# Performance work log

Measured on AMD Instinct MI355X. Metric: run time of the kernel, lower is better.

Reference implementation:

```python
import jax, jax.numpy as jnp
import numpy as np

T = 5
EPS = 1e-05
G = 4      # num_groups
D = 64     # num_channels per group


def setup_inputs() -> dict:
    key = jax.random.key(0)
    X = jax.random.normal(key, (32, 256, 56, 56), dtype=jnp.float32)
    weight = jnp.ones((1, 256, 1, 1), dtype=jnp.float32)
    bias = jnp.zeros((1, 256, 1, 1), dtype=jnp.float32)
    return {"X": X, "weight": weight, "bias": bias}


def reference(X, weight, bias):
    N, C, H, W = X.shape
    # (N,C,H,W) -> (C,N,H,W) -> (g, d, m) with m = N*H*W
    x = X.transpose(1, 0, 2, 3).reshape(G, D, -1)
    m = x.shape[-1]
    mean = x.mean(-1, keepdims=True)                 # (g, d, 1)
    xc = x - mean
    I = jnp.eye(D, dtype=X.dtype)
    # Sigma = eps*I + xc xc^T / m     (g, d, d)
    Sigma = EPS * I + jnp.einsum('gdm,gem->gde', xc, xc) / m
    # trace normalization
    rTr = 1.0 / jnp.trace(Sigma, axis1=1, axis2=2)[:, None, None]  # (g,1,1)
    Sn = Sigma * rTr
    # Newton-Schulz iterations: P_{k+1} = 1.5 P_k - 0.5 P_k^3 Sn
    P = jnp.broadcast_to(I, (G, D, D))
    for _ in range(T):
        P = 1.5 * P - 0.5 * (P @ P @ P @ Sn)
    wm = P * jnp.sqrt(rTr)                           # whitening matrix (g,d,d)
    xn = wm @ xc                                     # (g, d, m)
    Xh = xn.reshape(C, N, H, W).transpose(1, 0, 2, 3)
    return Xh * weight + bias
```

## Files before the change

kernel.cpp:

```cpp
#include <hip/hip_runtime.h>
#include <math.h>

#define GROUPS 4
#define DCH    64
#define NBATCH 32
#define CTOT   256
#define HW     3136
#define CHW    (CTOT*HW)
#define MTOT   (NBATCH*HW)
#define PB     196
#define EPSV   1e-5f

typedef __attribute__((ext_vector_type(8))) short bf16x8;
typedef __attribute__((ext_vector_type(4))) float f32x4;

__device__ __forceinline__ f32x4 mfma16(bf16x8 a, bf16x8 b, f32x4 c) {
    return __builtin_amdgcn_mfma_f32_16x16x32_bf16(a, b, c, 0, 0, 0);
}

__device__ __forceinline__ void split2(float x, short& h, short& l) {
    union { float f; unsigned u; } c; c.f = x;
    h = (short)(c.u >> 16);
    union { unsigned u; float f; } hm; hm.u = c.u & 0xFFFF0000u;
    union { float f; unsigned u; } lo; lo.f = x - hm.f;
    l = (short)(lo.u >> 16);
}

__device__ __forceinline__ void load_slab(const float* bp, float dst[16]) {
    float4 a0 = *reinterpret_cast<const float4*>(bp);
    float4 a1 = *reinterpret_cast<const float4*>(bp + 4);
    float4 b0 = *reinterpret_cast<const float4*>(bp + 32);
    float4 b1 = *reinterpret_cast<const float4*>(bp + 36);
    dst[0]=a0.x; dst[1]=a0.y; dst[2]=a0.z;  dst[3]=a0.w;
    dst[4]=a1.x; dst[5]=a1.y; dst[6]=a1.z;  dst[7]=a1.w;
    dst[8]=b0.x; dst[9]=b0.y; dst[10]=b0.z; dst[11]=b0.w;
    dst[12]=b1.x; dst[13]=b1.y; dst[14]=b1.z; dst[15]=b1.w;
}

__global__ __launch_bounds__(512) void k1_gram(const float* __restrict__ X,
                                               float* __restrict__ pGram,
                                               float* __restrict__ pSum)
{
    constexpr int KPB = MTOT / PB;
    constexpr int NST = KPB / 128;
    const int pb   = blockIdx.x;
    const int g    = blockIdx.y;
    const int tid  = threadIdx.x;
    const int w    = tid >> 6;
    const int lane = tid & 63;
    const int tr   = w & 3;
    const int par  = w >> 2;
    const int lr   = lane & 15;
    const int q    = lane >> 4;

    __shared__ float smem[8192];
    __shared__ float rsum[2][64];

    f32x4 acc[4];
#pragma unroll
    for (int c = 0; c < 4; ++c) acc[c] = (f32x4)(0.f);
    float sumv = 0.f;

    const float* Xg  = X + (size_t)g * DCH * HW;
    const int    row = 16 * tr + lr;

    float xv[3][16];
#pragma unroll
    for (int t0 = 0; t0 < 2; ++t0) {
        const int kk = pb * KPB + t0 * 128 + par * 64;
        const int n  = kk / HW;
        const int s  = kk - n * HW;
        load_slab(Xg + (size_t)n * CHW + (size_t)row * HW + s + q * 8, xv[t0]);
    }

#pragma unroll
    for (int t = 0; t < NST; ++t) {
        if (t + 2 < NST) {
            const int kk = pb * KPB + (t + 2) * 128 + par * 64;
            const int n  = kk / HW;
            const int s  = kk - n * HW;
            load_slab(Xg + (size_t)n * CHW + (size_t)row * HW + s + q * 8,
                      xv[(t + 2) % 3]);
        }
        __builtin_amdgcn_sched_barrier(0);
        bf16x8 ah[2], al[2];
#pragma unroll
        for (int ks = 0; ks < 2; ++ks) {
#pragma unroll
            for (int j = 0; j < 8; ++j) {
                float x = xv[t % 3][ks * 8 + j];
                sumv += x;
                short h, l; split2(x, h, l);
                ah[ks][j] = h; al[ks][j] = l;
            }
        }
#pragma unroll
        for (int ks = 0; ks < 2; ++ks) {
            *reinterpret_cast<bf16x8*>(&smem[(((par*4+tr)*2+ks)*2+0)*256 + lane*4]) = ah[ks];
            *reinterpret_cast<bf16x8*>(&smem[(((par*4+tr)*2+ks)*2+1)*256 + lane*4]) = al[ks];
        }
        __syncthreads();
#pragma unroll
        for (int c = 0; c < 4; ++c) {
#pragma unroll
            for (int ks = 0; ks < 2; ++ks) {
                bf16x8 bh = *reinterpret_cast<const bf16x8*>(
                    &smem[(((par*4+c)*2+ks)*2+0)*256 + lane*4]);
                bf16x8 bl = *reinterpret_cast<const bf16x8*>(
                    &smem[(((par*4+c)*2+ks)*2+1)*256 + lane*4]);
                acc[c] = mfma16(ah[ks], bh, acc[c]);
                acc[c] = mfma16(ah[ks], bl, acc[c]);
                acc[c] = mfma16(al[ks], bh, acc[c]);
            }
        }
        __syncthreads();
    }

    sumv += __shfl_xor(sumv, 16);
    sumv += __shfl_xor(sumv, 32);
    if (q == 0) rsum[par][row] = sumv;

#pragma unroll
    for (int c = 0; c < 4; ++c) {
#pragma unroll
        for (int r = 0; r < 4; ++r) {
            smem[par * 4096 + (16 * tr + 4 * q + r) * 64 + 16 * c + lr] = acc[c][r];
        }
    }
    __syncthreads();

    float* pg = pGram + ((size_t)g * PB + pb) * 4096;
    for (int i = tid; i < 4096; i += 512) pg[i] = smem[i] + smem[4096 + i];
    if (tid < 64)
        pSum[((size_t)g * PB + pb) * 64 + tid] = rsum[0][tid] + rsum[1][tid];
}

__global__ __launch_bounds__(256) void k2a1(const float* __restrict__ pGram,
                                            const float* __restrict__ pSum,
                                            float* __restrict__ pG2,
                                            float* __restrict__ pS2)
{
    constexpr int SLICE = PB / 7;
    const int cb  = blockIdx.x;
    const int g   = blockIdx.y;
    const int s   = blockIdx.z;
    const int tid = threadIdx.x;
    const int e = tid & 63, q = tid >> 6;
    __shared__ float red[4][64];
    __shared__ float red2[4][64];

    const float* pg = pGram + ((size_t)g * PB + s * SLICE + q) * 4096 + cb * 64 + e;
    float sum = 0.f;
#pragma unroll
    for (int i = 0; i < SLICE / 4; ++i)
        sum += pg[(size_t)i * 4 * 4096];
    red[q][e] = sum;
    if (cb == 0) {
        const float* ps = pSum + ((size_t)g * PB + s * SLICE + q) * 64 + e;
        float s2 = 0.f;
#pragma unroll
        for (int i = 0; i < SLICE / 4; ++i)
            s2 += ps[i * 4 * 64];
        red2[q][e] = s2;
    }
    __syncthreads();
    if (tid < 64) {
        pG2[((size_t)g * 7 + s) * 4096 + cb * 64 + tid] =
            red[0][tid] + red[1][tid] + red[2][tid] + red[3][tid];
        if (cb == 0)
            pS2[((size_t)g * 7 + s) * 64 + tid] =
                red2[0][tid] + red2[1][tid] + red2[2][tid] + red2[3][tid];
    }
}

__device__ __forceinline__ void packrow2(const float* __restrict__ M, int row, int q,
                                         bf16x8& h0, bf16x8& l0,
                                         bf16x8& h1, bf16x8& l1)
{
    const float* p = M + row * 68 + 8 * q;
    float4 a0 = *reinterpret_cast<const float4*>(p);
    float4 a1 = *reinterpret_cast<const float4*>(p + 4);
    float4 b0 = *reinterpret_cast<const float4*>(p + 32);
    float4 b1 = *reinterpret_cast<const float4*>(p + 36);
    float e0[8] = {a0.x, a0.y, a0.z, a0.w, a1.x, a1.y, a1.z, a1.w};
    float e1[8] = {b0.x, b0.y, b0.z, b0.w, b1.x, b1.y, b1.z, b1.w};
#pragma unroll
    for (int j = 0; j < 8; ++j) {
        short h, l;
        split2(e0[j], h, l); h0[j] = h; l0[j] = l;
        split2(e1[j], h, l); h1[j] = h; l1[j] = l;
    }
}

__global__ __launch_bounds__(256) void k2b_ns(const float* __restrict__ pG2,
                                              const float* __restrict__ pS2,
                                              const float* __restrict__ Wt,
                                              const float* __restrict__ Bs,
                                              float* __restrict__ Aout,
                                              float* __restrict__ Off)
{
    const int g   = blockIdx.x;
    const int tid = threadIdx.x;
    const int w = tid >> 6, lane = tid & 63, lr = lane & 15, q = lane >> 4;
    __shared__ float MP[64 * 68];
    __shared__ float MA[64 * 68];
    __shared__ float MB2[64 * 68];
    __shared__ float MS[64 * 68];
    __shared__ float lmean[64];
    __shared__ float redm[1024];
    __shared__ float rtr_s;

    if (tid < 64) {
        float s2 = 0.f;
#pragma unroll
        for (int s = 0; s < 7; ++s) s2 += pS2[((size_t)g * 7 + s) * 64 + tid];
        lmean[tid] = s2 * (1.0f / (float)MTOT);
    }
    __syncthreads();
    for (int idx = tid; idx < 4096; idx += 256) {
        int d = idx >> 6, e = idx & 63;
        float sum = 0.f;
#pragma unroll
        for (int s = 0; s < 7; ++s) sum += pG2[((size_t)g * 7 + s) * 4096 + idx];
        float v = sum * (1.0f / (float)MTOT) - lmean[d] * lmean[e];
        if (d == e) v += EPSV;
        MS[d * 68 + e] = v;
    }
    __syncthreads();
    if (tid < 64) {
        float v = MS[tid * 68 + tid];
#pragma unroll
        for (int off = 32; off > 0; off >>= 1) v += __shfl_down(v, off);
        if (tid == 0) rtr_s = 1.f / v;
    }
    __syncthreads();
    const float rTr = rtr_s;
    for (int idx = tid; idx < 4096; idx += 256) {
        int d = idx >> 6, e = idx & 63;
        float sv = MS[d * 68 + e] * rTr;
        MS[d * 68 + e] = sv;
        MP[d * 68 + e] = ((d == e) ? 1.5f : 0.f) - 0.5f * sv;
    }
    __syncthreads();

    bf16x8 snh0[4], snl0[4], snh1[4], snl1[4];
#pragma unroll
    for (int c = 0; c < 4; ++c)
        packrow2(MS, 16 * c + lr, q, snh0[c], snl0[c], snh1[c], snl1[c]);

    const int row_o = 16 * w + 4 * q;
    for (int it = 0; it < 4; ++it) {
        f32x4 a2[4], aS[4];
#pragma unroll
        for (int c = 0; c < 4; ++c) { a2[c] = (f32x4)(0.f); aS[c] = (f32x4)(0.f); }
        bf16x8 pah0, pal0, pah1, pal1;
        packrow2(MP, 16 * w + lr, q, pah0, pal0, pah1, pal1);
#pragma unroll
        for (int c = 0; c < 4; ++c) {
            bf16x8 bh0, bl0, bh1, bl1;
            packrow2(MP, 16 * c + lr, q, bh0, bl0, bh1, bl1);
            a2[c] = mfma16(pah0, bh0, a2[c]);
            a2[c] = mfma16(pah0, bl0, a2[c]);
            a2[c] = mfma16(pal0, bh0, a2[c]);
            a2[c] = mfma16(pah1, bh1, a2[c]);
            a2[c] = mfma16(pah1, bl1, a2[c]);
            a2[c] = mfma16(pal1, bh1, a2[c]);
            aS[c] = mfma16(pah0, snh0[c], aS[c]);
            aS[c] = mfma16(pah0, snl0[c], aS[c]);
            aS[c] = mfma16(pal0, snh0[c], aS[c]);
            aS[c] = mfma16(pah1, snh1[c], aS[c]);
            aS[c] = mfma16(pah1, snl1[c], aS[c]);
            aS[c] = mfma16(pal1, snh1[c], aS[c]);
        }
#pragma unroll
        for (int c = 0; c < 4; ++c)
#pragma unroll
            for (int r = 0; r < 4; ++r) {
                MA [(row_o + r) * 68 + 16 * c + lr] = a2[c][r];
                MB2[(row_o + r) * 68 + 16 * c + lr] = aS[c][r];
            }
        __syncthreads();

        f32x4 acc[4];
#pragma unroll
        for (int c = 0; c < 4; ++c) acc[c] = (f32x4)(0.f);
        bf16x8 qah0, qal0, qah1, qal1;
        packrow2(MA, 16 * w + lr, q, qah0, qal0, qah1, qal1);
#pragma unroll
        for (int c = 0; c < 4; ++c) {
            bf16x8 bh0, bl0, bh1, bl1;
            packrow2(MB2, 16 * c + lr, q, bh0, bl0, bh1, bl1);
            acc[c] = mfma16(qah0, bh0, acc[c]);
            acc[c] = mfma16(qah0, bl0, acc[c]);
            acc[c] = mfma16(qal0, bh0, acc[c]);
            acc[c] = mfma16(qah1, bh1, acc[c]);
            acc[c] = mfma16(qah1, bl1, acc[c]);
            acc[c] = mfma16(qal1, bh1, acc[c]);
        }
#pragma unroll
        for (int c = 0; c < 4; ++c)
#pragma unroll
            for (int r = 0; r < 4; ++r) {
                int o = (row_o + r) * 68 + 16 * c + lr;
                MP[o] = 1.5f * MP[o] - 0.5f * acc[c][r];
            }
        __syncthreads();
    }

    const float sc = sqrtf(rTr);
    const int i0 = (tid >> 4) << 2, j0 = (tid & 15) << 2;
#pragma unroll
    for (int i = 0; i < 4; ++i) {
        int d = i0 + i;
        float wv = Wt[g * 64 + d] * sc;
        float4 v;
        v.x = MP[d * 68 + j0 + 0] * wv;
        v.y = MP[d * 68 + j0 + 1] * wv;
        v.z = MP[d * 68 + j0 + 2] * wv;
        v.w = MP[d * 68 + j0 + 3] * wv;
        *reinterpret_cast<float4*>(Aout + g * 4096 + (d << 6) + j0) = v;
        redm[(d << 4) + (tid & 15)] =
            v.x * lmean[j0] + v.y * lmean[j0 + 1] + v.z * lmean[j0 + 2] + v.w * lmean[j0 + 3];
    }
    __syncthreads();
    if (tid < 64) {
        float s = 0.f;
#pragma unroll
        for (int qq = 0; qq < 16; ++qq) s += redm[(tid << 4) + qq];
        Off[g * 64 + tid] = Bs[g * 64 + tid] - s;
    }
}

__global__ __launch_bounds__(256) void k3_apply(const float* __restrict__ X,
                                                const float* __restrict__ Aout,
                                                const float* __restrict__ Off,
                                                float* __restrict__ Y)
{
    const int c    = blockIdx.x;
    const int g    = blockIdx.y;
    const int tid  = threadIdx.x;
    const int w    = tid >> 6;
    const int lane = tid & 63;
    const int lr   = lane & 15;
    const int q    = lane >> 4;

    const int col0 = c * 64;
    const int n    = col0 / HW;
    const int s0   = col0 - n * HW;
    const float* Xg   = X + (size_t)g * DCH * HW;
    const float* base = Xg + (size_t)n * CHW + s0 + 4 * lr;

    float4 xv[16];
#pragma unroll
    for (int ks = 0; ks < 2; ++ks)
#pragma unroll
        for (int j8 = 0; j8 < 8; ++j8)
            xv[ks * 8 + j8] =
                *reinterpret_cast<const float4*>(base + (size_t)(32 * ks + 8 * q + j8) * HW);

    bf16x8 ah[2], al[2];
#pragma unroll
    for (int s = 0; s < 2; ++s) {
        const float* ap = Aout + g * 4096 + (16 * w + lr) * 64 + 32 * s + 8 * q;
        float4 v0 = *reinterpret_cast<const float4*>(ap);
        float4 v1 = *reinterpret_cast<const float4*>(ap + 4);
        float av[8] = {v0.x, v0.y, v0.z, v0.w, v1.x, v1.y, v1.z, v1.w};
#pragma unroll
        for (int j = 0; j < 8; ++j) {
            short h, l; split2(av[j], h, l);
            ah[s][j] = h; al[s][j] = l;
        }
    }
    float offv[4];
#pragma unroll
    for (int r = 0; r < 4; ++r) offv[r] = Off[g * 64 + 16 * w + 4 * q + r];
    __builtin_amdgcn_sched_barrier(0);

    f32x4 accg[4];
#pragma unroll
    for (int j = 0; j < 4; ++j) accg[j] = (f32x4)(0.f);

#pragma unroll
    for (int ks = 0; ks < 2; ++ks) {
        bf16x8 bh[4], bl[4];
#pragma unroll
        for (int j8 = 0; j8 < 8; ++j8) {
            float4 v = xv[ks * 8 + j8];
            float vv[4] = {v.x, v.y, v.z, v.w};
#pragma unroll
            for (int jj = 0; jj < 4; ++jj) {
                short h, l; split2(vv[jj], h, l);
                bh[jj][j8] = h; bl[jj][j8] = l;
            }
        }
#pragma unroll
        for (int jj = 0; jj < 4; ++jj) {
            accg[jj] = mfma16(ah[ks], bh[jj], accg[jj]);
            accg[jj] = mfma16(ah[ks], bl[jj], accg[jj]);
            accg[jj] = mfma16(al[ks], bh[jj], accg[jj]);
        }
    }

    float* yp = Y + (size_t)g * DCH * HW + (size_t)n * CHW + s0 + 4 * lr;
#pragma unroll
    for (int r = 0; r < 4; ++r) {
        int row = 16 * w + 4 * q + r;
        float4 o;
        o.x = accg[0][r] + offv[r];
        o.y = accg[1][r] + offv[r];
        o.z = accg[2][r] + offv[r];
        o.w = accg[3][r] + offv[r];
        *reinterpret_cast<float4*>(yp + (size_t)row * HW) = o;
    }
}

extern "C" void kernel_launch(void* const* d_in, const int* in_sizes, int n_in,
                              void* d_out, int out_size, void* d_ws, size_t ws_size,
                              hipStream_t stream)
{
    const float* X  = (const float*)d_in[0];
    const float* Wt = (const float*)d_in[1];
    const float* Bs = (const float*)d_in[2];
    float* Y  = (float*)d_out;
    float* ws = (float*)d_ws;

    float* pGram = ws;
    float* pSum  = pGram + (size_t)4 * PB * 4096;
    float* pG2   = pSum  + (size_t)4 * PB * 64;
    float* pS2   = pG2   + (size_t)4 * 7 * 4096;
    float* Aout  = pS2   + (size_t)4 * 7 * 64;
    float* Off   = Aout  + 4 * 4096;

    k1_gram <<<dim3(PB, GROUPS), 512, 0, stream>>>(X, pGram, pSum);
    k2a1    <<<dim3(64, GROUPS, 7), 256, 0, stream>>>(pGram, pSum, pG2, pS2);
    k2b_ns  <<<dim3(GROUPS), 256, 0, stream>>>(pG2, pS2, Wt, Bs, Aout, Off);
    k3_apply<<<dim3(1568, GROUPS), 256, 0, stream>>>(X, Aout, Off, Y);
}
```

Measured before the change: 83.80 us.

## Reduce Gram prefetch depth and remap apply kernel to per-column MFMA tiles

```diff
diff --git a/kernel.cpp b/kernel.cpp
--- a/kernel.cpp
+++ b/kernel.cpp
@@ -64,31 +64,29 @@
     const float* Xg  = X + (size_t)g * DCH * HW;
     const int    row = 16 * tr + lr;
 
-    float xv[3][16];
-#pragma unroll
-    for (int t0 = 0; t0 < 2; ++t0) {
-        const int kk = pb * KPB + t0 * 128 + par * 64;
+    float xv[2][16];
+    {
+        const int kk = pb * KPB + par * 64;
         const int n  = kk / HW;
         const int s  = kk - n * HW;
-        load_slab(Xg + (size_t)n * CHW + (size_t)row * HW + s + q * 8, xv[t0]);
+        load_slab(Xg + (size_t)n * CHW + (size_t)row * HW + s + q * 8, xv[0]);
     }
 
 #pragma unroll
     for (int t = 0; t < NST; ++t) {
-        if (t + 2 < NST) {
-            const int kk = pb * KPB + (t + 2) * 128 + par * 64;
+        if (t + 1 < NST) {
+            const int kk = pb * KPB + (t + 1) * 128 + par * 64;
             const int n  = kk / HW;
             const int s  = kk - n * HW;
             load_slab(Xg + (size_t)n * CHW + (size_t)row * HW + s + q * 8,
-                      xv[(t + 2) % 3]);
-        }
-        __builtin_amdgcn_sched_barrier(0);
+                      xv[(t + 1) & 1]);
+        }
         bf16x8 ah[2], al[2];
 #pragma unroll
         for (int ks = 0; ks < 2; ++ks) {
 #pragma unroll
             for (int j = 0; j < 8; ++j) {
-                float x = xv[t % 3][ks * 8 + j];
+                float x = xv[t & 1][ks * 8 + j];
                 sumv += x;
                 short h, l; split2(x, h, l);
                 ah[ks][j] = h; al[ks][j] = l;
@@ -348,70 +346,68 @@
     const int n    = col0 / HW;
     const int s0   = col0 - n * HW;
     const float* Xg   = X + (size_t)g * DCH * HW;
-    const float* base = Xg + (size_t)n * CHW + s0 + 4 * lr;
-
-    float4 xv[16];
+    const float* base = Xg + (size_t)n * CHW + s0 + 16 * w + lr;
+
+    float xv[16];
 #pragma unroll
     for (int ks = 0; ks < 2; ++ks)
 #pragma unroll
         for (int j8 = 0; j8 < 8; ++j8)
-            xv[ks * 8 + j8] =
-                *reinterpret_cast<const float4*>(base + (size_t)(32 * ks + 8 * q + j8) * HW);
-
-    bf16x8 ah[2], al[2];
-#pragma unroll
-    for (int s = 0; s < 2; ++s) {
-        const float* ap = Aout + g * 4096 + (16 * w + lr) * 64 + 32 * s + 8 * q;
-        float4 v0 = *reinterpret_cast<const float4*>(ap);
-        float4 v1 = *reinterpret_cast<const float4*>(ap + 4);
-        float av[8] = {v0.x, v0.y, v0.z, v0.w, v1.x, v1.y, v1.z, v1.w};
-#pragma unroll
-        for (int j = 0; j < 8; ++j) {
-            short h, l; split2(av[j], h, l);
-            ah[s][j] = h; al[s][j] = l;
-        }
-    }
-    float offv[4];
-#pragma unroll
-    for (int r = 0; r < 4; ++r) offv[r] = Off[g * 64 + 16 * w + 4 * q + r];
+            xv[ks * 8 + j8] = base[(size_t)(32 * ks + 8 * q + j8) * HW];
+
+    bf16x8 ah[4][2], al[4][2];
+#pragma unroll
+    for (int b = 0; b < 4; ++b) {
+#pragma unroll
+        for (int s = 0; s < 2; ++s) {
+            const float* ap = Aout + g * 4096 + (16 * b + lr) * 64 + 32 * s + 8 * q;
+            float4 v0 = *reinterpret_cast<const float4*>(ap);
+            float4 v1 = *reinterpret_cast<const float4*>(ap + 4);
+            float av[8] = {v0.x, v0.y, v0.z, v0.w, v1.x, v1.y, v1.z, v1.w};
+#pragma unroll
+            for (int j = 0; j < 8; ++j) {
+                short h, l; split2(av[j], h, l);
+                ah[b][s][j] = h; al[b][s][j] = l;
+            }
+        }
+    }
+    float offv[4][4];
+#pragma unroll
+    for (int b = 0; b < 4; ++b)
+#pragma unroll
+        for (int r = 0; r < 4; ++r)
+            offv[b][r] = Off[g * 64 + 16 * b + 4 * q + r];
     __builtin_amdgcn_sched_barrier(0);
 
-    f32x4 accg[4];
-#pragma unroll
-    for (int j = 0; j < 4; ++j) accg[j] = (f32x4)(0.f);
-
+    bf16x8 bh[2], bl[2];
 #pragma unroll
     for (int ks = 0; ks < 2; ++ks) {
-        bf16x8 bh[4], bl[4];
 #pragma unroll
         for (int j8 = 0; j8 < 8; ++j8) {
-            float4 v = xv[ks * 8 + j8];
-            float vv[4] = {v.x, v.y, v.z, v.w};
-#pragma unroll
-            for (int jj = 0; jj < 4; ++jj) {
-                short h, l; split2(vv[jj], h, l);
-                bh[jj][j8] = h; bl[jj][j8] = l;
-            }
-        }
-#pragma unroll
-        for (int jj = 0; jj < 4; ++jj) {
-            accg[jj] = mfma16(ah[ks], bh[jj], accg[jj]);
-            accg[jj] = mfma16(ah[ks], bl[jj], accg[jj]);
-            accg[jj] = mfma16(al[ks], bh[jj], accg[jj]);
-        }
-    }
-
-    float* yp = Y + (size_t)g * DCH * HW + (size_t)n * CHW + s0 + 4 * lr;
-#pragma unroll
-    for (int r = 0; r < 4; ++r) {
-        int row = 16 * w + 4 * q + r;
-        float4 o;
-        o.x = accg[0][r] + offv[r];
-        o.y = accg[1][r] + offv[r];
-        o.z = accg[2][r] + offv[r];
-        o.w = accg[3][r] + offv[r];
-        *reinterpret_cast<float4*>(yp + (size_t)row * HW) = o;
-    }
+            short h, l; split2(xv[ks * 8 + j8], h, l);
+            bh[ks][j8] = h; bl[ks][j8] = l;
+        }
+    }
+
+    f32x4 acc[4];
+#pragma unroll
+    for (int b = 0; b < 4; ++b) acc[b] = (f32x4)(0.f);
+#pragma unroll
+    for (int b = 0; b < 4; ++b) {
+#pragma unroll
+        for (int ks = 0; ks < 2; ++ks) {
+            acc[b] = mfma16(ah[b][ks], bh[ks], acc[b]);
+            acc[b] = mfma16(ah[b][ks], bl[ks], acc[b]);
+            acc[b] = mfma16(al[b][ks], bh[ks], acc[b]);
+        }
+    }
+
+    float* yp = Y + (size_t)g * DCH * HW + (size_t)n * CHW + s0 + 16 * w + lr;
+#pragma unroll
+    for (int b = 0; b < 4; ++b)
+#pragma unroll
+        for (int r = 0; r < 4; ++r)
+            yp[(size_t)(16 * b + 4 * q + r) * HW] = acc[b][r] + offv[b][r];
 }
 
 extern "C" void kernel_launch(void* const* d_in, const int* in_sizes, int n_in,
```

New measurement: 109.0 us. +30.0%, slower.
